# Performance work log

Hardware: AMD Instinct MI355X
Metric: run time of the kernel (lower is better)

The kernel has to match this reference:

```python
import jax, jax.numpy as jnp
import numpy as np

N = 150000   # nonempty octree nodes at this depth
CIN = 256
CB = 64      # bottleneck channels = out_channels / bottleneck
COUT = 256
G = 32       # group-norm groups
K = 27       # 3x3x3 neighborhood
EPS = 1e-5


def group_norm(x, gamma, beta, groups=G):
    # x: [N, C]; octree GN treats the N nodes as the spatial extent of one instance
    n, c = x.shape
    xg = x.reshape(n, groups, c // groups)
    mu = xg.mean(axis=(0, 2), keepdims=True)
    var = xg.var(axis=(0, 2), keepdims=True)
    xg = (xg - mu) * jax.lax.rsqrt(var + EPS)
    return xg.reshape(n, c) * gamma + beta


def setup_inputs() -> dict:
    key = jax.random.key(0)
    ks = jax.random.split(key, 5)
    return {
        "data": jax.random.normal(ks[0], (N, CIN), jnp.float32),
        "neigh": jax.random.randint(ks[1], (N, K), 0, N, jnp.int32),
        "w1a": jax.random.normal(ks[2], (CIN, CB), jnp.float32) * 0.05,
        "g1a": jnp.ones((CB,), jnp.float32),
        "b1a": jnp.zeros((CB,), jnp.float32),
        "w3": jax.random.normal(ks[3], (K, CB, CB), jnp.float32) * 0.05,
        "g3": jnp.ones((CB,), jnp.float32),
        "b3": jnp.zeros((CB,), jnp.float32),
        "w1b": jax.random.normal(ks[4], (CB, COUT), jnp.float32) * 0.05,
        "g1b": jnp.ones((COUT,), jnp.float32),
        "b1b": jnp.zeros((COUT,), jnp.float32),
    }


def reference(data, neigh, w1a, g1a, b1a, w3, g3, b3, w1b, g1b, b1b):
    # conv1x1a + GN + ReLU
    x = jax.nn.relu(group_norm(data @ w1a, g1a, b1a))
    # octree 3x3x3 sparse conv: gather 27 neighbors, GEMM against [27,CB,CB] kernel
    gathered = x[neigh]                      # [N, 27, CB]
    y = jnp.einsum('nkc,kcd->nd', gathered, w3)
    y = jax.nn.relu(group_norm(y, g3, b3))
    # conv1x1b + GN
    z = group_norm(y @ w1b, g1b, b1b)
    # residual add (in_channels == out_channels -> identity skip) + ReLU
    return jax.nn.relu(z + data)
```

## Files before the change

kernel.cpp:

```cpp
#include <hip/hip_runtime.h>
#include <math.h>

#define CIN 256
#define CB 64
#define COUT 256
#define KNB 27
#define EPS 1e-5f

typedef unsigned short u16;
typedef __attribute__((ext_vector_type(8))) short short8;
typedef __attribute__((ext_vector_type(4))) float f32x4;

typedef const __attribute__((address_space(1))) unsigned int* gas_u32p;
typedef __attribute__((address_space(3))) unsigned int* las_u32p;
#define GLL(g, p) __builtin_amdgcn_global_load_lds((gas_u32p)(const void*)(g), \
        (las_u32p)(void*)(p), 16, 0, 0)

__device__ inline short f2bf(float f) {
    union { float f; unsigned u; } v; v.f = f;
    unsigned r = v.u + 0x7fff + ((v.u >> 16) & 1);
    return (short)(r >> 16);
}
__device__ inline float bf2f(short s) {
    union { unsigned u; float f; } v; v.u = ((unsigned)(u16)s) << 16;
    return v.f;
}
__device__ inline short8 pack8(float4 x0, float4 x1) {
    short8 r;
    r[0] = f2bf(x0.x); r[1] = f2bf(x0.y); r[2] = f2bf(x0.z); r[3] = f2bf(x0.w);
    r[4] = f2bf(x1.x); r[5] = f2bf(x1.y); r[6] = f2bf(x1.z); r[7] = f2bf(x1.w);
    return r;
}

__global__ void k_prep(const float* __restrict__ w1a, const float* __restrict__ w3,
                       const float* __restrict__ w1b, u16* __restrict__ w1at,
                       u16* __restrict__ w3img, u16* __restrict__ w1bt)
{
    int i = blockIdx.x * 256 + threadIdx.x;
    if (i < 16384) {
        int k = i >> 6, d = i & 63;
        w1at[d * 256 + k] = (u16)f2bf(w1a[i]);
    } else if (i < 126976) {
        int j = i - 16384;
        int k = j >> 12, c = (j >> 6) & 63, d = j & 63;
        w3img[(size_t)k * 4096 + d * 64 + (c ^ ((d & 7) << 3))] = (u16)f2bf(w3[j]);
    } else if (i < 143360) {
        int j = i - 126976;
        int c = j >> 8, d = j & 255;
        w1bt[d * 64 + c] = (u16)f2bf(w1b[j]);
    }
}

__global__ __launch_bounds__(256) void k_gemm1(const float* __restrict__ data,
        const u16* __restrict__ w1at, u16* __restrict__ t1,
        float* __restrict__ stats, int n)
{
    __shared__ float s_sum[32], s_sq[32];
    const int tid = threadIdx.x;
    if (tid < 32) { s_sum[tid] = 0.f; s_sq[tid] = 0.f; }
    __syncthreads();
    const int l = tid & 63, wv = tid >> 6;
    const int ll = l & 15, lh = l >> 4;
    const int rowbase = blockIdx.x * 256 + wv * 64;

    f32x4 acc[4][4] = {};
#pragma unroll
    for (int kc = 0; kc < 8; ++kc) {
        short8 b[4];
#pragma unroll
        for (int f = 0; f < 4; ++f)
            b[f] = *(const short8*)(w1at + (size_t)(f * 16 + ll) * 256 + kc * 32 + lh * 8);
#pragma unroll
        for (int rt = 0; rt < 4; ++rt) {
            int row = rowbase + rt * 16 + ll;
            int rowc = (row < n) ? row : 0;
            const float* ar = data + (size_t)rowc * CIN + kc * 32 + lh * 8;
            short8 a = pack8(*(const float4*)ar, *(const float4*)(ar + 4));
#pragma unroll
            for (int f = 0; f < 4; ++f)
                acc[rt][f] = __builtin_amdgcn_mfma_f32_16x16x32_bf16(a, b[f], acc[rt][f], 0, 0, 0);
        }
    }
    float gs[4] = {0.f, 0.f, 0.f, 0.f}, gq[4] = {0.f, 0.f, 0.f, 0.f};
#pragma unroll
    for (int rt = 0; rt < 4; ++rt) {
#pragma unroll
        for (int f = 0; f < 4; ++f) {
#pragma unroll
            for (int r = 0; r < 4; ++r) {
                int rr = rowbase + rt * 16 + lh * 4 + r;
                if (rr < n) {
                    float v = acc[rt][f][r];
                    t1[(size_t)rr * CB + f * 16 + ll] = (u16)f2bf(v);
                    gs[f] += v; gq[f] += v * v;
                }
            }
        }
    }
#pragma unroll
    for (int f = 0; f < 4; ++f) {
        float s = gs[f], q = gq[f];
        s += __shfl_xor(s, 1); s += __shfl_xor(s, 16); s += __shfl_xor(s, 32);
        q += __shfl_xor(q, 1); q += __shfl_xor(q, 16); q += __shfl_xor(q, 32);
        if ((l & 0x31) == 0) {
            atomicAdd(&s_sum[f * 8 + (ll >> 1)], s);
            atomicAdd(&s_sq [f * 8 + (ll >> 1)], q);
        }
    }
    __syncthreads();
    if (tid < 32) {
        atomicAdd(&stats[tid], s_sum[tid]);
        atomicAdd(&stats[32 + tid], s_sq[tid]);
    }
}

__global__ void k_apply64(u16* __restrict__ buf, const float* __restrict__ st,
        const float* __restrict__ gamma, const float* __restrict__ beta, int n)
{
    const float cnt = (float)n * 2.0f;
    const int total = n * 8;
    for (int i = blockIdx.x * blockDim.x + threadIdx.x; i < total;
         i += gridDim.x * blockDim.x) {
        int c0 = (i & 7) * 8;
        short8 v = ((short8*)buf)[i];
#pragma unroll
        for (int j = 0; j < 8; ++j) {
            int c = c0 + j, g = c >> 1;
            float mu = st[g] / cnt;
            float var = st[32 + g] / cnt - mu * mu;
            float inv = rsqrtf(var + EPS);
            float x = bf2f(v[j]);
            x = fmaxf((x - mu) * inv * gamma[c] + beta[c], 0.f);
            v[j] = f2bf(x);
        }
        ((short8*)buf)[i] = v;
    }
}

__global__ __launch_bounds__(256, 4) void k_conv(const u16* __restrict__ xb,
        const int* __restrict__ neigh, const u16* __restrict__ w3img,
        u16* __restrict__ y, float* __restrict__ stats, int n)
{
    __shared__ u16 s_w3[2][8192];
    __shared__ float s_sum[32], s_sq[32];
    const int tid = threadIdx.x;
    if (tid < 32) { s_sum[tid] = 0.f; s_sq[tid] = 0.f; }
    const int row0 = blockIdx.x * 128;
    const int l = tid & 63, wv = tid >> 6;
    const int ll = l & 15, lh = l >> 4;
    const int r0 = row0 + wv * 32 + ll;
    const int r1 = r0 + 16;
    const int* __restrict__ nrow0 = neigh + (size_t)((r0 < n) ? r0 : 0) * KNB;
    const int* __restrict__ nrow1 = neigh + (size_t)((r1 < n) ? r1 : 0) * KNB;
    const int so  = wv * 2048 + l * 8;
    const int so1 = wv * 1024 + l * 8;

    short8 A[3][4];
    int ixa[3], ixb[3];

    ixa[0] = nrow0[0]; ixb[0] = nrow1[0];
    ixa[1] = nrow0[1]; ixb[1] = nrow1[1];
    __builtin_amdgcn_sched_barrier(0);
#pragma unroll
    for (int j = 0; j < 4; ++j)
        GLL(w3img + so + j * 512, &s_w3[0][0] + so + j * 512);
    __builtin_amdgcn_sched_barrier(0);
    {
        const u16* xa = xb + (size_t)ixa[0] * CB + lh * 8;
        const u16* xc = xb + (size_t)ixb[0] * CB + lh * 8;
        A[0][0] = *(const short8*)xa; A[0][1] = *(const short8*)(xa + 32);
        A[0][2] = *(const short8*)xc; A[0][3] = *(const short8*)(xc + 32);
    }
    {
        const u16* xa = xb + (size_t)ixa[1] * CB + lh * 8;
        const u16* xc = xb + (size_t)ixb[1] * CB + lh * 8;
        A[1][0] = *(const short8*)xa; A[1][1] = *(const short8*)(xa + 32);
        A[1][2] = *(const short8*)xc; A[1][3] = *(const short8*)(xc + 32);
    }
    ixa[2] = nrow0[2]; ixb[2] = nrow1[2];
    ixa[0] = nrow0[3]; ixb[0] = nrow1[3];
    asm volatile("s_waitcnt vmcnt(12) lgkmcnt(0)" ::: "memory");
    __builtin_amdgcn_s_barrier();
    __builtin_amdgcn_sched_barrier(0);

    f32x4 acc[2][4] = {};
#pragma unroll
    for (int c = 0; c < 14; ++c) {
        const int buf = c & 1;
        const int npg = (c < 13) ? 2 : 1;
        if (c < 13) {
            if (c + 1 < 13) {
                const u16* gsrc = w3img + (size_t)(c + 1) * 8192 + so;
                u16* ldst = &s_w3[buf ^ 1][0] + so;
#pragma unroll
                for (int j = 0; j < 4; ++j)
                    GLL(gsrc + j * 512, ldst + j * 512);
            } else {
                const u16* gsrc = w3img + (size_t)(c + 1) * 8192 + so1;
                u16* ldst = &s_w3[buf ^ 1][0] + so1;
#pragma unroll
                for (int j = 0; j < 2; ++j)
                    GLL(gsrc + j * 512, ldst + j * 512);
            }
        }
        __builtin_amdgcn_sched_barrier(0);
#pragma unroll
        for (int s = 0; s < 2; ++s) {
            if (s >= npg) continue;
            const int k = c * 2 + s;
            if (k + 4 <= 26) {
                ixa[(k + 4) % 3] = nrow0[k + 4];
                ixb[(k + 4) % 3] = nrow1[k + 4];
            }
            __builtin_amdgcn_sched_barrier(0);
            if (k + 2 <= 26) {
                const u16* xa = xb + (size_t)ixa[(k + 2) % 3] * CB + lh * 8;
                const u16* xc = xb + (size_t)ixb[(k + 2) % 3] * CB + lh * 8;
                A[(k + 2) % 3][0] = *(const short8*)xa;
                A[(k + 2) % 3][1] = *(const short8*)(xa + 32);
                A[(k + 2) % 3][2] = *(const short8*)xc;
                A[(k + 2) % 3][3] = *(const short8*)(xc + 32);
            }
            __builtin_amdgcn_sched_barrier(0);
            const char* bpage = (const char*)&s_w3[buf][0] + s * 8192;
#pragma unroll
            for (int f = 0; f < 4; ++f) {
                int d = f * 16 + ll;
                int swz = (d & 7) << 4;
                short8 b0 = *(const short8*)(bpage + d * 128 + ((lh * 16) ^ swz));
                short8 b1 = *(const short8*)(bpage + d * 128 + ((64 + lh * 16) ^ swz));
                acc[0][f] = __builtin_amdgcn_mfma_f32_16x16x32_bf16(A[k % 3][0], b0, acc[0][f], 0, 0, 0);
                acc[0][f] = __builtin_amdgcn_mfma_f32_16x16x32_bf16(A[k % 3][1], b1, acc[0][f], 0, 0, 0);
                acc[1][f] = __builtin_amdgcn_mfma_f32_16x16x32_bf16(A[k % 3][2], b0, acc[1][f], 0, 0, 0);
                acc[1][f] = __builtin_amdgcn_mfma_f32_16x16x32_bf16(A[k % 3][3], b1, acc[1][f], 0, 0, 0);
            }
        }
        if (c <= 10)
            asm volatile("s_waitcnt vmcnt(12) lgkmcnt(0)" ::: "memory");
        else if (c == 11)
            asm volatile("s_waitcnt vmcnt(10) lgkmcnt(0)" ::: "memory");
        else if (c == 12)
            asm volatile("s_waitcnt vmcnt(4) lgkmcnt(0)" ::: "memory");
        if (c < 13) {
            __builtin_amdgcn_s_barrier();
            __builtin_amdgcn_sched_barrier(0);
        }
    }

    float gs[4] = {0.f, 0.f, 0.f, 0.f}, gq[4] = {0.f, 0.f, 0.f, 0.f};
#pragma unroll
    for (int rt = 0; rt < 2; ++rt) {
#pragma unroll
        for (int f = 0; f < 4; ++f) {
#pragma unroll
            for (int r = 0; r < 4; ++r) {
                int rr = row0 + wv * 32 + rt * 16 + lh * 4 + r;
                if (rr < n) {
                    float v = acc[rt][f][r];
                    y[(size_t)rr * CB + f * 16 + ll] = (u16)f2bf(v);
                    gs[f] += v; gq[f] += v * v;
                }
            }
        }
    }
#pragma unroll
    for (int f = 0; f < 4; ++f) {
        float s = gs[f], q = gq[f];
        s += __shfl_xor(s, 1); s += __shfl_xor(s, 16); s += __shfl_xor(s, 32);
        q += __shfl_xor(q, 1); q += __shfl_xor(q, 16); q += __shfl_xor(q, 32);
        if ((l & 0x31) == 0) {
            atomicAdd(&s_sum[f * 8 + (ll >> 1)], s);
            atomicAdd(&s_sq [f * 8 + (ll >> 1)], q);
        }
    }
    __syncthreads();
    if (tid < 32) {
        atomicAdd(&stats[64 + tid], s_sum[tid]);
        atomicAdd(&stats[96 + tid], s_sq[tid]);
    }
}

__global__ __launch_bounds__(256) void k_gemm2(const u16* __restrict__ y2,
        const u16* __restrict__ w1bt, float* __restrict__ z, u16* __restrict__ zb,
        float* __restrict__ stats, const float* __restrict__ g3,
        const float* __restrict__ b3, int n)
{
    __shared__ float s_sum[8], s_sq[8];
    const int tid = threadIdx.x;
    if (tid < 8) { s_sum[tid] = 0.f; s_sq[tid] = 0.f; }
    __syncthreads();
    const int l = tid & 63, wv = tid >> 6;
    const int ll = l & 15, lh = l >> 4;
    const int rowbase = blockIdx.x * 256 + wv * 64;
    const int cb = blockIdx.y;

    const float* st2 = stats + 64;
    const float cnt2 = (float)n * 2.0f;
    float sc[16], sh[16];
#pragma unroll
    for (int j = 0; j < 16; ++j) {
        int c = (j < 8) ? (lh * 8 + j) : (32 + lh * 8 + (j - 8));
        int g = c >> 1;
        float mu = st2[g] / cnt2;
        float var = st2[32 + g] / cnt2 - mu * mu;
        float inv = rsqrtf(var + EPS);
        float gm = g3[c];
        sc[j] = inv * gm;
        sh[j] = b3[c] - mu * inv * gm;
    }

    short8 b0[4], b1[4];
#pragma unroll
    for (int f = 0; f < 4; ++f) {
        const u16* br = w1bt + (size_t)(cb * 64 + f * 16 + ll) * CB + lh * 8;
        b0[f] = *(const short8*)(br);
        b1[f] = *(const short8*)(br + 32);
    }
    f32x4 acc[4][4] = {};
#pragma unroll
    for (int rt = 0; rt < 4; ++rt) {
        int row = rowbase + rt * 16 + ll;
        int rowc = (row < n) ? row : 0;
        const u16* ar = y2 + (size_t)rowc * CB + lh * 8;
        short8 r0 = *(const short8*)(ar);
        short8 r1 = *(const short8*)(ar + 32);
        short8 a0, a1;
#pragma unroll
        for (int j = 0; j < 8; ++j) {
            a0[j] = f2bf(fmaxf(bf2f(r0[j]) * sc[j] + sh[j], 0.f));
            a1[j] = f2bf(fmaxf(bf2f(r1[j]) * sc[8 + j] + sh[8 + j], 0.f));
        }
#pragma unroll
        for (int f = 0; f < 4; ++f) {
            acc[rt][f] = __builtin_amdgcn_mfma_f32_16x16x32_bf16(a0, b0[f], acc[rt][f], 0, 0, 0);
            acc[rt][f] = __builtin_amdgcn_mfma_f32_16x16x32_bf16(a1, b1[f], acc[rt][f], 0, 0, 0);
        }
    }
    float gs[4] = {0.f, 0.f, 0.f, 0.f}, gq[4] = {0.f, 0.f, 0.f, 0.f};
#pragma unroll
    for (int rt = 0; rt < 4; ++rt) {
#pragma unroll
        for (int f = 0; f < 4; ++f) {
#pragma unroll
            for (int r = 0; r < 4; ++r) {
                int rr = rowbase + rt * 16 + lh * 4 + r;
                if (rr < n) {
                    float v = acc[rt][f][r];
                    size_t off = (size_t)rr * COUT + cb * 64 + f * 16 + ll;
                    if (zb) zb[off] = (u16)f2bf(v); else z[off] = v;
                    gs[f] += v; gq[f] += v * v;
                }
            }
        }
    }
#pragma unroll
    for (int f = 0; f < 4; ++f) {
        float s = gs[f], q = gq[f];
        s += __shfl_xor(s, 1); s += __shfl_xor(s, 2); s += __shfl_xor(s, 4);
        s += __shfl_xor(s, 16); s += __shfl_xor(s, 32);
        q += __shfl_xor(q, 1); q += __shfl_xor(q, 2); q += __shfl_xor(q, 4);
        q += __shfl_xor(q, 16); q += __shfl_xor(q, 32);
        if ((l & 0x37) == 0) {
            atomicAdd(&s_sum[f * 2 + (ll >> 3)], s);
            atomicAdd(&s_sq [f * 2 + (ll >> 3)], q);
        }
    }
    __syncthreads();
    if (tid < 8) {
        atomicAdd(&stats[128 + cb * 8 + tid], s_sum[tid]);
        atomicAdd(&stats[160 + cb * 8 + tid], s_sq[tid]);
    }
}

__global__ void k_final_bf(float* __restrict__ out, const u16* __restrict__ zb,
        const float* __restrict__ data, const float* __restrict__ st,
        const float* __restrict__ gamma, const float* __restrict__ beta, int n)
{
    const float cnt = (float)n * 8.0f;
    const int total = n * 32;
    for (int i = blockIdx.x * blockDim.x + threadIdx.x; i < total;
         i += gridDim.x * blockDim.x) {
        int c0 = (i & 31) * 8;
        int g = c0 >> 3;
        float mu = st[g] / cnt;
        float var = st[32 + g] / cnt - mu * mu;
        float inv = rsqrtf(var + EPS);
        short8 zv = ((const short8*)zb)[i];
        float dd[8], oo[8];
        *(float4*)dd = *(const float4*)(data + (size_t)i * 8);
        *(float4*)(dd + 4) = *(const float4*)(data + (size_t)i * 8 + 4);
#pragma unroll
        for (int j = 0; j < 8; ++j)
            oo[j] = fmaxf((bf2f(zv[j]) - mu) * inv * gamma[c0 + j] + beta[c0 + j] + dd[j], 0.f);
        *(float4*)(out + (size_t)i * 8) = *(float4*)oo;
        *(float4*)(out + (size_t)i * 8 + 4) = *(float4*)(oo + 4);
    }
}

__global__ void k_final(float* __restrict__ zo, const float* __restrict__ data,
        const float* __restrict__ st, const float* __restrict__ gamma,
        const float* __restrict__ beta, int n)
{
    const float cnt = (float)n * 8.0f;
    const int total = n * (COUT / 4);
    for (int i = blockIdx.x * blockDim.x + threadIdx.x; i < total;
         i += gridDim.x * blockDim.x) {
        int c4 = (i & (COUT / 4 - 1)) * 4;
        int g = c4 >> 3;
        float mu = st[g] / cnt;
        float var = st[32 + g] / cnt - mu * mu;
        float inv = rsqrtf(var + EPS);
        float4 zv = *(float4*)(zo + (size_t)i * 4);
        float4 dv = *(const float4*)(data + (size_t)i * 4);
        zv.x = fmaxf((zv.x - mu) * inv * gamma[c4 + 0] + beta[c4 + 0] + dv.x, 0.f);
        zv.y = fmaxf((zv.y - mu) * inv * gamma[c4 + 1] + beta[c4 + 1] + dv.y, 0.f);
        zv.z = fmaxf((zv.z - mu) * inv * gamma[c4 + 2] + beta[c4 + 2] + dv.z, 0.f);
        zv.w = fmaxf((zv.w - mu) * inv * gamma[c4 + 3] + beta[c4 + 3] + dv.w, 0.f);
        *(float4*)(zo + (size_t)i * 4) = zv;
    }
}

extern "C" void kernel_launch(void* const* d_in, const int* in_sizes, int n_in,
                              void* d_out, int out_size, void* d_ws, size_t ws_size,
                              hipStream_t stream)
{
    const float* data = (const float*)d_in[0];
    const int*   neigh = (const int*)d_in[1];
    const float* w1a = (const float*)d_in[2];
    const float* g1a = (const float*)d_in[3];
    const float* b1a = (const float*)d_in[4];
    const float* w3  = (const float*)d_in[5];
    const float* g3  = (const float*)d_in[6];
    const float* b3  = (const float*)d_in[7];
    const float* w1b = (const float*)d_in[8];
    const float* g1b = (const float*)d_in[9];
    const float* b1b = (const float*)d_in[10];
    float* out = (float*)d_out;
    float* ws  = (float*)d_ws;

    const int n = in_sizes[0] / CIN;

    float* stats = ws;
    u16* w1at  = (u16*)(ws + 256);
    u16* w3img = w1at + 16384;
    u16* w1bt  = w3img + 110592;
    u16* t1    = w1bt + 16384;
    u16* ybuf  = t1 + (size_t)n * CB;
    u16* zb    = nullptr;
    {
        size_t need = 1024 + 286720 + (size_t)n * CB * 4 + (size_t)n * COUT * 2;
        if (ws_size >= need) zb = ybuf + (size_t)n * CB;
    }

    hipMemsetAsync(stats, 0, 192 * sizeof(float), stream);

    const int nb128 = (n + 127) / 128;
    const int nb256 = (n + 255) / 256;
    k_prep<<<560, 256, 0, stream>>>(w1a, w3, w1b, w1at, w3img, w1bt);
    k_gemm1<<<nb256, 256, 0, stream>>>(data, w1at, t1, stats, n);
    k_apply64<<<2048, 256, 0, stream>>>(t1, stats, g1a, b1a, n);
    k_conv<<<nb128, 256, 0, stream>>>(t1, neigh, w3img, ybuf, stats, n);
    k_gemm2<<<dim3(nb256, 4), 256, 0, stream>>>(ybuf, w1bt, out, zb, stats, g3, b3, n);
    if (zb)
        k_final_bf<<<2048, 256, 0, stream>>>(out, zb, data, stats + 128, g1b, b1b, n);
    else
        k_final<<<2048, 256, 0, stream>>>(out, data, stats + 128, g1b, b1b, n);
}
```

Before: 290.0 us.

## Fuse GN1 apply into conv gather and recompute final GEMM instead of storing z

Removes the standalone GN1 apply pass by applying the normalize+ReLU to gathered neighbor rows inside the conv kernel, which redoes that work 27 times per row. Replaces the gemm2 plus final pass that wrote and reread the 256-channel z buffer with a stats-only GEMM pass and a second pass that recomputes the small 64x256 GEMM and applies GN, the residual and ReLU directly into the output. This trades extra MFMA and ALU work for less HBM traffic on the large intermediate. The conv launch bound drops to 3 waves per SIMD to make room for the extra registers.

```diff
diff --git a/kernel.cpp b/kernel.cpp
--- a/kernel.cpp
+++ b/kernel.cpp
@@ -114,32 +114,10 @@
     }
 }
 
-__global__ void k_apply64(u16* __restrict__ buf, const float* __restrict__ st,
-        const float* __restrict__ gamma, const float* __restrict__ beta, int n)
-{
-    const float cnt = (float)n * 2.0f;
-    const int total = n * 8;
-    for (int i = blockIdx.x * blockDim.x + threadIdx.x; i < total;
-         i += gridDim.x * blockDim.x) {
-        int c0 = (i & 7) * 8;
-        short8 v = ((short8*)buf)[i];
-#pragma unroll
-        for (int j = 0; j < 8; ++j) {
-            int c = c0 + j, g = c >> 1;
-            float mu = st[g] / cnt;
-            float var = st[32 + g] / cnt - mu * mu;
-            float inv = rsqrtf(var + EPS);
-            float x = bf2f(v[j]);
-            x = fmaxf((x - mu) * inv * gamma[c] + beta[c], 0.f);
-            v[j] = f2bf(x);
-        }
-        ((short8*)buf)[i] = v;
-    }
-}
-
-__global__ __launch_bounds__(256, 4) void k_conv(const u16* __restrict__ xb,
+__global__ __launch_bounds__(256, 3) void k_conv(const u16* __restrict__ xb,
         const int* __restrict__ neigh, const u16* __restrict__ w3img,
-        u16* __restrict__ y, float* __restrict__ stats, int n)
+        u16* __restrict__ y, float* __restrict__ stats,
+        const float* __restrict__ g1a, const float* __restrict__ b1a, int n)
 {
     __shared__ u16 s_w3[2][8192];
     __shared__ float s_sum[32], s_sq[32];
@@ -155,6 +133,23 @@
     const int so  = wv * 2048 + l * 8;
     const int so1 = wv * 1024 + l * 8;
 
+    const float cnt1 = (float)n * 2.0f;
+    float sc1[16], sh1[16];
+#pragma unroll
+    for (int j = 0; j < 16; ++j) {
+        int c = (j < 8) ? (lh * 8 + j) : (32 + lh * 8 + (j - 8));
+        int g = c >> 1;
+        float mu = stats[g] / cnt1;
+        float var = stats[32 + g] / cnt1 - mu * mu;
+        float inv = rsqrtf(var + EPS);
+        float gm = g1a[c];
+        sc1[j] = inv * gm;
+        sh1[j] = b1a[c] - mu * inv * gm;
+    }
+    __builtin_amdgcn_sched_barrier(0);
+    asm volatile("s_waitcnt vmcnt(0)" ::: "memory");
+    __builtin_amdgcn_sched_barrier(0);
+
     short8 A[3][4];
     int ixa[3], ixb[3];
 
@@ -222,6 +217,14 @@
                 A[(k + 2) % 3][3] = *(const short8*)(xc + 32);
             }
             __builtin_amdgcn_sched_barrier(0);
+            short8 a0, a1, a2, a3;
+#pragma unroll
+            for (int j = 0; j < 8; ++j) {
+                a0[j] = f2bf(fmaxf(bf2f(A[k % 3][0][j]) * sc1[j]     + sh1[j],     0.f));
+                a1[j] = f2bf(fmaxf(bf2f(A[k % 3][1][j]) * sc1[8 + j] + sh1[8 + j], 0.f));
+                a2[j] = f2bf(fmaxf(bf2f(A[k % 3][2][j]) * sc1[j]     + sh1[j],     0.f));
+                a3[j] = f2bf(fmaxf(bf2f(A[k % 3][3][j]) * sc1[8 + j] + sh1[8 + j], 0.f));
+            }
             const char* bpage = (const char*)&s_w3[buf][0] + s * 8192;
 #pragma unroll
             for (int f = 0; f < 4; ++f) {
@@ -229,10 +232,10 @@
                 int swz = (d & 7) << 4;
                 short8 b0 = *(const short8*)(bpage + d * 128 + ((lh * 16) ^ swz));
                 short8 b1 = *(const short8*)(bpage + d * 128 + ((64 + lh * 16) ^ swz));
-                acc[0][f] = __builtin_amdgcn_mfma_f32_16x16x32_bf16(A[k % 3][0], b0, acc[0][f], 0, 0, 0);
-                acc[0][f] = __builtin_amdgcn_mfma_f32_16x16x32_bf16(A[k % 3][1], b1, acc[0][f], 0, 0, 0);
-                acc[1][f] = __builtin_amdgcn_mfma_f32_16x16x32_bf16(A[k % 3][2], b0, acc[1][f], 0, 0, 0);
-                acc[1][f] = __builtin_amdgcn_mfma_f32_16x16x32_bf16(A[k % 3][3], b1, acc[1][f], 0, 0, 0);
+                acc[0][f] = __builtin_amdgcn_mfma_f32_16x16x32_bf16(a0, b0, acc[0][f], 0, 0, 0);
+                acc[0][f] = __builtin_amdgcn_mfma_f32_16x16x32_bf16(a1, b1, acc[0][f], 0, 0, 0);
+                acc[1][f] = __builtin_amdgcn_mfma_f32_16x16x32_bf16(a2, b0, acc[1][f], 0, 0, 0);
+                acc[1][f] = __builtin_amdgcn_mfma_f32_16x16x32_bf16(a3, b1, acc[1][f], 0, 0, 0);
             }
         }
         if (c <= 10)
@@ -280,19 +283,17 @@
     }
 }
 
-__global__ __launch_bounds__(256) void k_gemm2(const u16* __restrict__ y2,
-        const u16* __restrict__ w1bt, float* __restrict__ z, u16* __restrict__ zb,
-        float* __restrict__ stats, const float* __restrict__ g3,
-        const float* __restrict__ b3, int n)
-{
-    __shared__ float s_sum[8], s_sq[8];
+__global__ __launch_bounds__(256) void k_gemm2s(const u16* __restrict__ y2,
+        const u16* __restrict__ w1bt, float* __restrict__ stats,
+        const float* __restrict__ g3, const float* __restrict__ b3, int n)
+{
+    __shared__ float s_sum[32], s_sq[32];
     const int tid = threadIdx.x;
-    if (tid < 8) { s_sum[tid] = 0.f; s_sq[tid] = 0.f; }
+    if (tid < 32) { s_sum[tid] = 0.f; s_sq[tid] = 0.f; }
     __syncthreads();
     const int l = tid & 63, wv = tid >> 6;
     const int ll = l & 15, lh = l >> 4;
-    const int rowbase = blockIdx.x * 256 + wv * 64;
-    const int cb = blockIdx.y;
+    const int rowbase = blockIdx.x * 128 + wv * 32;
 
     const float* st2 = stats + 64;
     const float cnt2 = (float)n * 2.0f;
@@ -308,115 +309,147 @@
         sc[j] = inv * gm;
         sh[j] = b3[c] - mu * inv * gm;
     }
-
-    short8 b0[4], b1[4];
-#pragma unroll
-    for (int f = 0; f < 4; ++f) {
-        const u16* br = w1bt + (size_t)(cb * 64 + f * 16 + ll) * CB + lh * 8;
-        b0[f] = *(const short8*)(br);
-        b1[f] = *(const short8*)(br + 32);
-    }
-    f32x4 acc[4][4] = {};
-#pragma unroll
-    for (int rt = 0; rt < 4; ++rt) {
+    short8 A0[2], A1[2];
+#pragma unroll
+    for (int rt = 0; rt < 2; ++rt) {
         int row = rowbase + rt * 16 + ll;
         int rowc = (row < n) ? row : 0;
         const u16* ar = y2 + (size_t)rowc * CB + lh * 8;
         short8 r0 = *(const short8*)(ar);
         short8 r1 = *(const short8*)(ar + 32);
-        short8 a0, a1;
 #pragma unroll
         for (int j = 0; j < 8; ++j) {
-            a0[j] = f2bf(fmaxf(bf2f(r0[j]) * sc[j] + sh[j], 0.f));
-            a1[j] = f2bf(fmaxf(bf2f(r1[j]) * sc[8 + j] + sh[8 + j], 0.f));
-        }
-#pragma unroll
-        for (int f = 0; f < 4; ++f) {
-            acc[rt][f] = __builtin_amdgcn_mfma_f32_16x16x32_bf16(a0, b0[f], acc[rt][f], 0, 0, 0);
-            acc[rt][f] = __builtin_amdgcn_mfma_f32_16x16x32_bf16(a1, b1[f], acc[rt][f], 0, 0, 0);
-        }
-    }
-    float gs[4] = {0.f, 0.f, 0.f, 0.f}, gq[4] = {0.f, 0.f, 0.f, 0.f};
-#pragma unroll
-    for (int rt = 0; rt < 4; ++rt) {
-#pragma unroll
-        for (int f = 0; f < 4; ++f) {
-#pragma unroll
-            for (int r = 0; r < 4; ++r) {
-                int rr = rowbase + rt * 16 + lh * 4 + r;
-                if (rr < n) {
-                    float v = acc[rt][f][r];
-                    size_t off = (size_t)rr * COUT + cb * 64 + f * 16 + ll;
-                    if (zb) zb[off] = (u16)f2bf(v); else z[off] = v;
-                    gs[f] += v; gq[f] += v * v;
+            A0[rt][j] = f2bf(fmaxf(bf2f(r0[j]) * sc[j] + sh[j], 0.f));
+            A1[rt][j] = f2bf(fmaxf(bf2f(r1[j]) * sc[8 + j] + sh[8 + j], 0.f));
+        }
+    }
+#pragma unroll
+    for (int cb = 0; cb < 4; ++cb) {
+        short8 b0[4], b1[4];
+#pragma unroll
+        for (int f = 0; f < 4; ++f) {
+            const u16* br = w1bt + (size_t)(cb * 64 + f * 16 + ll) * CB + lh * 8;
+            b0[f] = *(const short8*)(br);
+            b1[f] = *(const short8*)(br + 32);
+        }
+        f32x4 acc[2][4] = {};
+#pragma unroll
+        for (int rt = 0; rt < 2; ++rt)
+#pragma unroll
+            for (int f = 0; f < 4; ++f) {
+                acc[rt][f] = __builtin_amdgcn_mfma_f32_16x16x32_bf16(A0[rt], b0[f], acc[rt][f], 0, 0, 0);
+                acc[rt][f] = __builtin_amdgcn_mfma_f32_16x16x32_bf16(A1[rt], b1[f], acc[rt][f], 0, 0, 0);
+            }
+#pragma unroll
+        for (int f = 0; f < 4; ++f) {
+            float gs = 0.f, gq = 0.f;
+#pragma unroll
+            for (int rt = 0; rt < 2; ++rt)
+#pragma unroll
+                for (int r = 0; r < 4; ++r) {
+                    int rr = rowbase + rt * 16 + lh * 4 + r;
+                    if (rr < n) {
+                        float v = acc[rt][f][r];
+                        gs += v; gq += v * v;
+                    }
                 }
-            }
-        }
-    }
-#pragma unroll
-    for (int f = 0; f < 4; ++f) {
-        float s = gs[f], q = gq[f];
-        s += __shfl_xor(s, 1); s += __shfl_xor(s, 2); s += __shfl_xor(s, 4);
-        s += __shfl_xor(s, 16); s += __shfl_xor(s, 32);
-        q += __shfl_xor(q, 1); q += __shfl_xor(q, 2); q += __shfl_xor(q, 4);
-        q += __shfl_xor(q, 16); q += __shfl_xor(q, 32);
-        if ((l & 0x37) == 0) {
-            atomicAdd(&s_sum[f * 2 + (ll >> 3)], s);
-            atomicAdd(&s_sq [f * 2 + (ll >> 3)], q);
+            gs += __shfl_xor(gs, 1); gs += __shfl_xor(gs, 2); gs += __shfl_xor(gs, 4);
+            gs += __shfl_xor(gs, 16); gs += __shfl_xor(gs, 32);
+            gq += __shfl_xor(gq, 1); gq += __shfl_xor(gq, 2); gq += __shfl_xor(gq, 4);
+            gq += __shfl_xor(gq, 16); gq += __shfl_xor(gq, 32);
+            if ((l & 0x37) == 0) {
+                atomicAdd(&s_sum[cb * 8 + f * 2 + (ll >> 3)], gs);
+                atomicAdd(&s_sq [cb * 8 + f * 2 + (ll >> 3)], gq);
+            }
         }
     }
     __syncthreads();
-    if (tid < 8) {
-        atomicAdd(&stats[128 + cb * 8 + tid], s_sum[tid]);
-        atomicAdd(&stats[160 + cb * 8 + tid], s_sq[tid]);
-    }
-}
-
-__global__ void k_final_bf(float* __restrict__ out, const u16* __restrict__ zb,
-        const float* __restrict__ data, const float* __restrict__ st,
-        const float* __restrict__ gamma, const float* __restrict__ beta, int n)
-{
-    const float cnt = (float)n * 8.0f;
-    const int total = n * 32;
-    for (int i = blockIdx.x * blockDim.x + threadIdx.x; i < total;
-         i += gridDim.x * blockDim.x) {
-        int c0 = (i & 31) * 8;
-        int g = c0 >> 3;
-        float mu = st[g] / cnt;
-        float var = st[32 + g] / cnt - mu * mu;
+    if (tid < 32) {
+        atomicAdd(&stats[128 + tid], s_sum[tid]);
+        atomicAdd(&stats[160 + tid], s_sq[tid]);
+    }
+}
+
+__global__ __launch_bounds__(256) void k_final2(const u16* __restrict__ y2,
+        const u16* __restrict__ w1bt, const float* __restrict__ data,
+        float* __restrict__ out, const float* __restrict__ stats,
+        const float* __restrict__ g3, const float* __restrict__ b3,
+        const float* __restrict__ g1b, const float* __restrict__ b1b, int n)
+{
+    const int tid = threadIdx.x;
+    const int l = tid & 63, wv = tid >> 6;
+    const int ll = l & 15, lh = l >> 4;
+    const int rowbase = blockIdx.x * 128 + wv * 32;
+
+    const float* st2 = stats + 64;
+    const float cnt2 = (float)n * 2.0f;
+    float sc[16], sh[16];
+#pragma unroll
+    for (int j = 0; j < 16; ++j) {
+        int c = (j < 8) ? (lh * 8 + j) : (32 + lh * 8 + (j - 8));
+        int g = c >> 1;
+        float mu = st2[g] / cnt2;
+        float var = st2[32 + g] / cnt2 - mu * mu;
         float inv = rsqrtf(var + EPS);
-        short8 zv = ((const short8*)zb)[i];
-        float dd[8], oo[8];
-        *(float4*)dd = *(const float4*)(data + (size_t)i * 8);
-        *(float4*)(dd + 4) = *(const float4*)(data + (size_t)i * 8 + 4);
-#pragma unroll
-        for (int j = 0; j < 8; ++j)
-            oo[j] = fmaxf((bf2f(zv[j]) - mu) * inv * gamma[c0 + j] + beta[c0 + j] + dd[j], 0.f);
-        *(float4*)(out + (size_t)i * 8) = *(float4*)oo;
-        *(float4*)(out + (size_t)i * 8 + 4) = *(float4*)(oo + 4);
-    }
-}
-
-__global__ void k_final(float* __restrict__ zo, const float* __restrict__ data,
-        const float* __restrict__ st, const float* __restrict__ gamma,
-        const float* __restrict__ beta, int n)
-{
-    const float cnt = (float)n * 8.0f;
-    const int total = n * (COUT / 4);
-    for (int i = blockIdx.x * blockDim.x + threadIdx.x; i < total;
-         i += gridDim.x * blockDim.x) {
-        int c4 = (i & (COUT / 4 - 1)) * 4;
-        int g = c4 >> 3;
-        float mu = st[g] / cnt;
-        float var = st[32 + g] / cnt - mu * mu;
-        float inv = rsqrtf(var + EPS);
-        float4 zv = *(float4*)(zo + (size_t)i * 4);
-        float4 dv = *(const float4*)(data + (size_t)i * 4);
-        zv.x = fmaxf((zv.x - mu) * inv * gamma[c4 + 0] + beta[c4 + 0] + dv.x, 0.f);
-        zv.y = fmaxf((zv.y - mu) * inv * gamma[c4 + 1] + beta[c4 + 1] + dv.y, 0.f);
-        zv.z = fmaxf((zv.z - mu) * inv * gamma[c4 + 2] + beta[c4 + 2] + dv.z, 0.f);
-        zv.w = fmaxf((zv.w - mu) * inv * gamma[c4 + 3] + beta[c4 + 3] + dv.w, 0.f);
-        *(float4*)(zo + (size_t)i * 4) = zv;
+        float gm = g3[c];
+        sc[j] = inv * gm;
+        sh[j] = b3[c] - mu * inv * gm;
+    }
+    short8 A0[2], A1[2];
+#pragma unroll
+    for (int rt = 0; rt < 2; ++rt) {
+        int row = rowbase + rt * 16 + ll;
+        int rowc = (row < n) ? row : 0;
+        const u16* ar = y2 + (size_t)rowc * CB + lh * 8;
+        short8 r0 = *(const short8*)(ar);
+        short8 r1 = *(const short8*)(ar + 32);
+#pragma unroll
+        for (int j = 0; j < 8; ++j) {
+            A0[rt][j] = f2bf(fmaxf(bf2f(r0[j]) * sc[j] + sh[j], 0.f));
+            A1[rt][j] = f2bf(fmaxf(bf2f(r1[j]) * sc[8 + j] + sh[8 + j], 0.f));
+        }
+    }
+    const float* st3 = stats + 128;
+    const float cnt3 = (float)n * 8.0f;
+#pragma unroll
+    for (int cb = 0; cb < 4; ++cb) {
+        short8 b0[4], b1[4];
+#pragma unroll
+        for (int f = 0; f < 4; ++f) {
+            const u16* br = w1bt + (size_t)(cb * 64 + f * 16 + ll) * CB + lh * 8;
+            b0[f] = *(const short8*)(br);
+            b1[f] = *(const short8*)(br + 32);
+        }
+        f32x4 acc[2][4] = {};
+#pragma unroll
+        for (int rt = 0; rt < 2; ++rt)
+#pragma unroll
+            for (int f = 0; f < 4; ++f) {
+                acc[rt][f] = __builtin_amdgcn_mfma_f32_16x16x32_bf16(A0[rt], b0[f], acc[rt][f], 0, 0, 0);
+                acc[rt][f] = __builtin_amdgcn_mfma_f32_16x16x32_bf16(A1[rt], b1[f], acc[rt][f], 0, 0, 0);
+            }
+#pragma unroll
+        for (int f = 0; f < 4; ++f) {
+            int c = cb * 64 + f * 16 + ll;
+            int g = c >> 3;
+            float mu = st3[g] / cnt3;
+            float var = st3[32 + g] / cnt3 - mu * mu;
+            float inv = rsqrtf(var + EPS);
+            float gm = g1b[c];
+            float sc3 = inv * gm;
+            float sh3 = b1b[c] - mu * inv * gm;
+#pragma unroll
+            for (int rt = 0; rt < 2; ++rt)
+#pragma unroll
+                for (int r = 0; r < 4; ++r) {
+                    int rr = rowbase + rt * 16 + lh * 4 + r;
+                    if (rr < n) {
+                        size_t off = (size_t)rr * COUT + c;
+                        float o = acc[rt][f][r] * sc3 + sh3 + data[off];
+                        out[off] = fmaxf(o, 0.f);
+                    }
+                }
+        }
     }
 }
 
@@ -446,11 +479,6 @@
     u16* w1bt  = w3img + 110592;
     u16* t1    = w1bt + 16384;
     u16* ybuf  = t1 + (size_t)n * CB;
-    u16* zb    = nullptr;
-    {
-        size_t need = 1024 + 286720 + (size_t)n * CB * 4 + (size_t)n * COUT * 2;
-        if (ws_size >= need) zb = ybuf + (size_t)n * CB;
-    }
 
     hipMemsetAsync(stats, 0, 192 * sizeof(float), stream);
 
@@ -458,11 +486,7 @@
     const int nb256 = (n + 255) / 256;
     k_prep<<<560, 256, 0, stream>>>(w1a, w3, w1b, w1at, w3img, w1bt);
     k_gemm1<<<nb256, 256, 0, stream>>>(data, w1at, t1, stats, n);
-    k_apply64<<<2048, 256, 0, stream>>>(t1, stats, g1a, b1a, n);
-    k_conv<<<nb128, 256, 0, stream>>>(t1, neigh, w3img, ybuf, stats, n);
-    k_gemm2<<<dim3(nb256, 4), 256, 0, stream>>>(ybuf, w1bt, out, zb, stats, g3, b3, n);
-    if (zb)
-        k_final_bf<<<2048, 256, 0, stream>>>(out, zb, data, stats + 128, g1b, b1b, n);
-    else
-        k_final<<<2048, 256, 0, stream>>>(out, data, stats + 128, g1b, b1b, n);
-}
+    k_conv<<<nb128, 256, 0, stream>>>(t1, neigh, w3img, ybuf, stats, g1a, b1a, n);
+    k_gemm2s<<<nb128, 256, 0, stream>>>(ybuf, w1bt, stats, g3, b3, n);
+    k_final2<<<nb128, 256, 0, stream>>>(ybuf, w1bt, data, out, stats, g3, b3, g1b, b1b, n);
+}
```

Measured after the change: 383.9 us. 32.3% more time.
